# Kernel optimization log

Measured on AMD Instinct MI355X. Metric: run time of the kernel, lower is better.

The kernel has to match this reference:

```python
import jax, jax.numpy as jnp
import numpy as np

B, S, H = 32, 4096, 16
QC, LORA, ROPE, NOPE, VH, DM = 1536, 512, 64, 128, 128, 2048
SCALE = 1.0 / np.sqrt(NOPE + ROPE)


def _rope(x, pos):
    # GPT-NeoX style rotary, dim=ROPE, base=10000. x: [B,H,ROPE] or [B,ROPE]
    half = ROPE // 2
    inv = 1.0 / (10000.0 ** (jnp.arange(half, dtype=jnp.float32) / half))
    f = pos.astype(jnp.float32)[:, None] * inv  # [B, half]
    cos, sin = jnp.cos(f), jnp.sin(f)
    if x.ndim == 3:
        cos, sin = cos[:, None, :], sin[:, None, :]
    x1, x2 = x[..., :half], x[..., half:]
    return jnp.concatenate([x1 * cos - x2 * sin, x2 * cos + x1 * sin], axis=-1)


def setup_inputs() -> dict:
    key = jax.random.key(0)
    ks = jax.random.split(key, 11)
    w = 0.02  # small init so logits are well-scaled
    return {
        "q_c": jax.random.normal(ks[0], (B, QC), jnp.float32),
        "k_c_normed": jax.random.normal(ks[1], (B, LORA), jnp.float32),
        "k_pe": jax.random.normal(ks[2], (B, ROPE), jnp.float32),
        "kv_c_cache": jax.random.normal(ks[3], (B, S, LORA), jnp.float32),
        "k_pe_cache": jax.random.normal(ks[4], (B, S, ROPE), jnp.float32),
        "W_UQ": jax.random.normal(ks[5], (QC, H, NOPE), jnp.float32) * w,
        "W_UK": jax.random.normal(ks[6], (LORA, H, NOPE), jnp.float32) * w,
        "W_QR": jax.random.normal(ks[7], (QC, H * ROPE), jnp.float32) * w,
        "W_UV": jax.random.normal(ks[8], (LORA, H, VH), jnp.float32) * w,
        "W_O": jax.random.normal(ks[9], (H * VH, DM), jnp.float32) * w,
        "input_positions": jnp.full((B,), S - 1, dtype=jnp.int32),
    }


def reference(q_c, k_c_normed, k_pe, kv_c_cache, k_pe_cache,
              W_UQ, W_UK, W_QR, W_UV, W_O, input_positions):
    pos = input_positions
    # matrix-absorbed q_nope: (q_c @ W_UQ) absorbed through W_UK -> latent space
    q_t = jnp.einsum('bd,dhn->bhn', q_c, W_UQ)            # [B,H,NOPE]
    q_nope = jnp.einsum('bhn,lhn->bhl', q_t, W_UK)        # [B,H,LORA]
    q_pe = _rope((q_c @ W_QR).reshape(B, H, ROPE), pos)   # [B,H,ROPE]
    k_pe_rot = _rope(k_pe, pos)                            # [B,ROPE]
    # write current latent token into cache (paged write flattened)
    b_idx = jnp.arange(B)
    kv_c = kv_c_cache.at[b_idx, pos].set(k_c_normed)       # [B,S,LORA]
    kp = k_pe_cache.at[b_idx, pos].set(k_pe_rot)           # [B,S,ROPE]
    # attention in latent space
    scores = (jnp.einsum('bhl,bsl->bhs', q_nope, kv_c)
              + jnp.einsum('bhr,bsr->bhs', q_pe, kp)) * SCALE
    attn = jax.nn.softmax(scores, axis=-1)                 # [B,H,S]
    o = jnp.einsum('bhs,bsl->bhl', attn, kv_c)             # [B,H,LORA]
    v = jnp.einsum('bhl,lhv->bhv', o, W_UV)                # [B,H,VH]
    out = v.reshape(B, H * VH) @ W_O                       # [B,DM]
    return out.reshape(B, 1, DM)
```

## Files before the change

kernel.cpp:

```cpp
#include <hip/hip_runtime.h>
#include <hip/hip_bf16.h>
#include <math.h>

#define B 32
#define S 4096
#define H 16
#define QC 1536
#define LORA 512
#define ROPE 64
#define NOPE 128
#define VH 128
#define DM 2048
#define NC 32
#define CHUNK (S / NC)
#define TR 8
#define NT (CHUNK / TR)
#define NKS 24

__device__ __constant__ float SCALE_C = 0.07216878364870323f;

__global__ __launch_bounds__(256) void k_proj_part(
    const float* __restrict__ q_c, const float* __restrict__ W_UQ,
    const float* __restrict__ W_QR, float* __restrict__ part) {
    const int ks = blockIdx.x, cs = blockIdx.y, t = threadIdx.x;
    const int k0 = ks * 64;
    __shared__ float qs[64][32];
    for (int i = t; i < 64 * 32; i += 256) {
        const int k = i >> 5, b2 = i & 31;
        qs[k][b2] = q_c[(size_t)b2 * QC + k0 + k];
    }
    __syncthreads();
    const int tc = t & 63, tb = t >> 6;
    const int col = cs * 256 + tc * 4;
    const float* W; int N, coll;
    if (cs < 8) { W = W_UQ; N = 2048; coll = col; }
    else        { W = W_QR; N = 1024; coll = col - 2048; }
    float4 acc[8];
#pragma unroll
    for (int i = 0; i < 8; i++) acc[i] = make_float4(0.f, 0.f, 0.f, 0.f);
#pragma unroll 4
    for (int k = 0; k < 64; ++k) {
        const float4 w4 = *(const float4*)(W + (size_t)(k0 + k) * N + coll);
        const float4 a1 = *(const float4*)&qs[k][tb * 8];
        const float4 a2 = *(const float4*)&qs[k][tb * 8 + 4];
        acc[0].x += a1.x * w4.x; acc[0].y += a1.x * w4.y; acc[0].z += a1.x * w4.z; acc[0].w += a1.x * w4.w;
        acc[1].x += a1.y * w4.x; acc[1].y += a1.y * w4.y; acc[1].z += a1.y * w4.z; acc[1].w += a1.y * w4.w;
        acc[2].x += a1.z * w4.x; acc[2].y += a1.z * w4.y; acc[2].z += a1.z * w4.z; acc[2].w += a1.z * w4.w;
        acc[3].x += a1.w * w4.x; acc[3].y += a1.w * w4.y; acc[3].z += a1.w * w4.z; acc[3].w += a1.w * w4.w;
        acc[4].x += a2.x * w4.x; acc[4].y += a2.x * w4.y; acc[4].z += a2.x * w4.z; acc[4].w += a2.x * w4.w;
        acc[5].x += a2.y * w4.x; acc[5].y += a2.y * w4.y; acc[5].z += a2.y * w4.z; acc[5].w += a2.y * w4.w;
        acc[6].x += a2.z * w4.x; acc[6].y += a2.z * w4.y; acc[6].z += a2.z * w4.z; acc[6].w += a2.z * w4.w;
        acc[7].x += a2.w * w4.x; acc[7].y += a2.w * w4.y; acc[7].z += a2.w * w4.z; acc[7].w += a2.w * w4.w;
    }
#pragma unroll
    for (int j = 0; j < 8; j++) {
        const int b2 = tb * 8 + j;
        *(float4*)(part + ((size_t)ks * 32 + b2) * 3072 + col) = acc[j];
    }
}

__global__ void k_proj_reduce(const float* __restrict__ part, float* __restrict__ q_t,
                              float* __restrict__ qr) {
    const int idx = blockIdx.x * 256 + threadIdx.x;
    const int b = idx / 768, c4 = idx % 768;
    const int col = c4 * 4;
    float4 acc = make_float4(0.f, 0.f, 0.f, 0.f);
    for (int ks = 0; ks < NKS; ks++) {
        const float4 p = *(const float4*)(part + ((size_t)ks * 32 + b) * 3072 + col);
        acc.x += p.x; acc.y += p.y; acc.z += p.z; acc.w += p.w;
    }
    if (col < 2048) *(float4*)(q_t + (size_t)b * 2048 + col) = acc;
    else            *(float4*)(qr + (size_t)b * 1024 + col - 2048) = acc;
}

__global__ void k_rope(const float* __restrict__ qr, const float* __restrict__ k_pe,
                       const int* __restrict__ pos_arr, float* __restrict__ q_pe,
                       float* __restrict__ kpe_rot) {
    const int b = blockIdx.x, t = threadIdx.x;
    const int pos = pos_arr[b];
    for (int p = t; p < (H + 1) * 32; p += 256) {
        const int j = p & 31;
        const int grp = p >> 5;
        const double inv = pow(10000.0, -(double)j / 32.0);
        const double f = (double)pos * inv;
        const float c = (float)cos(f), s = (float)sin(f);
        if (grp < H) {
            const float* x = qr + (size_t)b * 1024 + grp * 64;
            float* o = q_pe + (size_t)b * 1024 + grp * 64;
            const float x1 = x[j], x2 = x[j + 32];
            o[j] = x1 * c - x2 * s;
            o[j + 32] = x2 * c + x1 * s;
        } else {
            const float* x = k_pe + (size_t)b * 64;
            float* o = kpe_rot + (size_t)b * 64;
            const float x1 = x[j], x2 = x[j + 32];
            o[j] = x1 * c - x2 * s;
            o[j + 32] = x2 * c + x1 * s;
        }
    }
}

__global__ __launch_bounds__(256) void k_qnope(
    const float* __restrict__ q_t, const float* __restrict__ W_UK,
    float* __restrict__ q_nope) {
    const int l0 = blockIdx.x * 64, b0 = blockIdx.y * 4, h = blockIdx.z;
    const int t = threadIdx.x;
    __shared__ float qs[4][NOPE];
    for (int i = t; i < 4 * NOPE; i += 256) {
        const int b2 = i >> 7, n = i & 127;
        qs[b2][n] = q_t[(size_t)(b0 + b2) * 2048 + h * NOPE + n];
    }
    __syncthreads();
    const int wave = t >> 6, lane = t & 63;
    const int half = lane >> 5, nl = (lane & 31) * 4;
    for (int sw = 0; sw < 8; ++sw) {
        const int l = l0 + sw * 8 + wave * 2 + half;
        const float4 w4 = *(const float4*)(W_UK + ((size_t)l * H + h) * NOPE + nl);
#pragma unroll
        for (int b2 = 0; b2 < 4; ++b2) {
            const float4 a4 = *(const float4*)&qs[b2][nl];
            float d = a4.x * w4.x + a4.y * w4.y + a4.z * w4.z + a4.w * w4.w;
            d += __shfl_xor(d, 16);
            d += __shfl_xor(d, 8);
            d += __shfl_xor(d, 4);
            d += __shfl_xor(d, 2);
            d += __shfl_xor(d, 1);
            if ((lane & 31) == 0)
                q_nope[((size_t)(b0 + b2) * H + h) * LORA + l] = d;
        }
    }
}

__global__ __launch_bounds__(256) void k_flash(
    const float* __restrict__ q_nope, const float* __restrict__ q_pe,
    const float* __restrict__ kv_cache, const float* __restrict__ kpe_cache,
    const float* __restrict__ k_c_normed, const float* __restrict__ kpe_rot,
    const int* __restrict__ pos_arr, float* __restrict__ part_o,
    float* __restrict__ part_ml) {
    __shared__ float lds_kv[2][TR][LORA];
    __shared__ float lds_pe[2][TR][ROPE];
    const int blk = blockIdx.x;
    const int b = blk / NC, c = blk % NC;
    const int t = threadIdx.x;
    const int g = t >> 4, j = t & 15;
    const int wave = t >> 6, lane = t & 63;
    const int pos = pos_arr[b];
    const int s0 = c * CHUNK;
    const int rel = pos - s0;
    const int ptile = (rel >= 0 && rel < CHUNK) ? (rel / TR) : -1;

    const char* kvg = (const char*)kv_cache + (size_t)b * S * LORA * 4;
    const char* peg = (const char*)kpe_cache + (size_t)b * S * ROPE * 4;
    const float* kc_b = k_c_normed + (size_t)b * LORA;
    const float* kr_b = kpe_rot + (size_t)b * ROPE;

    const int wo = wave * 1024 + lane * 16;

    auto stage = [&](int bi, int tile) {
        const char* gk = kvg + (size_t)(s0 + tile * TR) * (LORA * 4);
        char* lk = (char*)&lds_kv[bi][0][0];
#pragma unroll
        for (int i = 0; i < 4; ++i) {
            __builtin_amdgcn_global_load_lds(
                (const __attribute__((address_space(1))) void*)(gk + i * 4096 + wo),
                (__attribute__((address_space(3))) void*)(lk + i * 4096 + wave * 1024),
                16, 0, 0);
        }
        if (t < 128) {
            const char* gp = peg + (size_t)(s0 + tile * TR) * (ROPE * 4);
            char* lp = (char*)&lds_pe[bi][0][0];
            __builtin_amdgcn_global_load_lds(
                (const __attribute__((address_space(1))) void*)(gp + wo),
                (__attribute__((address_space(3))) void*)(lp + wave * 1024),
                16, 0, 0);
        }
    };
    auto patch = [&](int bi, int prow) {
        if (t < 128)
            ((float4*)&lds_kv[bi][prow][0])[t] = ((const float4*)kc_b)[t];
        else if (t < 144)
            ((float4*)&lds_pe[bi][prow][0])[t - 128] = ((const float4*)kr_b)[t - 128];
    };

    float4 q4[9];
    const float* qn = q_nope + ((size_t)b * H + g) * LORA;
#pragma unroll
    for (int k = 0; k < 8; k++) q4[k] = *(const float4*)(qn + 4 * j + 64 * k);
    q4[8] = *(const float4*)(q_pe + ((size_t)b * H + g) * 64 + 4 * j);

    float m_run = -INFINITY, l_run = 0.f;
    float4 o_acc[8];
#pragma unroll
    for (int k = 0; k < 8; k++) o_acc[k] = make_float4(0.f, 0.f, 0.f, 0.f);

    stage(0, 0);
    asm volatile("s_waitcnt vmcnt(0)" ::: "memory");
    __syncthreads();
    if (ptile == 0) { patch(0, rel); __syncthreads(); }

    int cur = 0;
    for (int tile = 0; tile < NT; ++tile) {
        if (tile + 1 < NT) stage(cur ^ 1, tile + 1);

        for (int r = 0; r < TR; ++r) {
            const float* kvr = &lds_kv[cur][r][0];
            float4 kv4[8];
#pragma unroll
            for (int k = 0; k < 8; k++) kv4[k] = *(const float4*)(kvr + 4 * j + 64 * k);
            float4 p4 = *(const float4*)(&lds_pe[cur][r][0] + 4 * j);

            float acc = 0.f;
#pragma unroll
            for (int k = 0; k < 8; k++)
                acc += q4[k].x * kv4[k].x + q4[k].y * kv4[k].y +
                       q4[k].z * kv4[k].z + q4[k].w * kv4[k].w;
            acc += q4[8].x * p4.x + q4[8].y * p4.y + q4[8].z * p4.z + q4[8].w * p4.w;
            acc += __shfl_xor(acc, 8);
            acc += __shfl_xor(acc, 4);
            acc += __shfl_xor(acc, 2);
            acc += __shfl_xor(acc, 1);
            const float sc = acc * SCALE_C;

            if (sc > m_run + 8.0f) {
                const float alpha = __expf(m_run - sc);
                l_run *= alpha;
#pragma unroll
                for (int k = 0; k < 8; k++) {
                    o_acc[k].x *= alpha; o_acc[k].y *= alpha;
                    o_acc[k].z *= alpha; o_acc[k].w *= alpha;
                }
                m_run = sc;
            }
            const float p = __expf(sc - m_run);
            l_run += p;
#pragma unroll
            for (int k = 0; k < 8; k++) {
                o_acc[k].x += p * kv4[k].x; o_acc[k].y += p * kv4[k].y;
                o_acc[k].z += p * kv4[k].z; o_acc[k].w += p * kv4[k].w;
            }
        }

        asm volatile("s_waitcnt vmcnt(0)" ::: "memory");
        __syncthreads();
        if (tile + 1 < NT && ptile == tile + 1) {
            patch(cur ^ 1, rel - ptile * TR);
            __syncthreads();
        }
        cur ^= 1;
    }

    float* po = part_o + (((size_t)b * NC + c) * H + g) * LORA;
#pragma unroll
    for (int k = 0; k < 8; k++) *(float4*)(po + 4 * j + 64 * k) = o_acc[k];
    if (j == 0) {
        float* pml = part_ml + (((size_t)b * NC + c) * H + g) * 2;
        pml[0] = m_run;
        pml[1] = l_run;
    }
}

__global__ __launch_bounds__(256) void k_combine(
    const float* __restrict__ part_o, const float* __restrict__ part_ml,
    const float* __restrict__ W_UV, float* __restrict__ v) {
    const int b0 = blockIdx.x * 4, h = blockIdx.y, t = threadIdx.x;
    __shared__ float ml_s[4][NC][2];
    __shared__ float o_s[4][LORA];
    if (t < 256) {
        const int b2 = t >> 6, c = (t >> 1) & 31, w = t & 1;
        ml_s[b2][c][w] = part_ml[(((size_t)(b0 + b2) * NC + c) * H + h) * 2 + w];
    }
    __syncthreads();
    float m_b[4], inv_l[4];
#pragma unroll
    for (int b2 = 0; b2 < 4; ++b2) {
        float m = -INFINITY;
        for (int c = 0; c < NC; c++) m = fmaxf(m, ml_s[b2][c][0]);
        float l = 0.f;
        for (int c = 0; c < NC; c++) l += ml_s[b2][c][1] * __expf(ml_s[b2][c][0] - m);
        m_b[b2] = m;
        inv_l[b2] = 1.0f / l;
    }
    for (int i = t; i < 4 * LORA; i += 256) {
        const int b2 = i >> 9, li = i & 511;
        float acc = 0.f;
        for (int c = 0; c < NC; c++) {
            acc += part_o[(((size_t)(b0 + b2) * NC + c) * H + h) * LORA + li] *
                   __expf(ml_s[b2][c][0] - m_b[b2]);
        }
        o_s[b2][li] = acc * inv_l[b2];
    }
    __syncthreads();
    const int vi = t & 127, bp = t >> 7;
    float acc0 = 0.f, acc1 = 0.f;
    for (int l = 0; l < LORA; l += 4) {
        const float w0 = W_UV[(size_t)(l + 0) * (H * VH) + h * VH + vi];
        const float w1 = W_UV[(size_t)(l + 1) * (H * VH) + h * VH + vi];
        const float w2 = W_UV[(size_t)(l + 2) * (H * VH) + h * VH + vi];
        const float w3 = W_UV[(size_t)(l + 3) * (H * VH) + h * VH + vi];
        const float4 oa = *(const float4*)&o_s[bp * 2][l];
        const float4 ob = *(const float4*)&o_s[bp * 2 + 1][l];
        acc0 += oa.x * w0 + oa.y * w1 + oa.z * w2 + oa.w * w3;
        acc1 += ob.x * w0 + ob.y * w1 + ob.z * w2 + ob.w * w3;
    }
    v[(size_t)(b0 + bp * 2) * (H * VH) + h * VH + vi] = acc0;
    v[(size_t)(b0 + bp * 2 + 1) * (H * VH) + h * VH + vi] = acc1;
}

__global__ void k_out(const float* __restrict__ v, const float* __restrict__ W_O,
                      float* __restrict__ out_part) {
    const int dsl = blockIdx.x, ksl = blockIdx.y, t = threadIdx.x;
    const int d0 = dsl * 128, k0 = ksl * 128;
    __shared__ float vs[32][128];
    for (int i = t; i < 32 * 128; i += 256) {
        const int bi = i >> 7, kk = i & 127;
        vs[bi][kk] = v[(size_t)bi * DM + k0 + kk];
    }
    __syncthreads();
    const int dl = t & 127, bh = t >> 7;
    float acc[16];
#pragma unroll
    for (int i = 0; i < 16; i++) acc[i] = 0.f;
    for (int kk = 0; kk < 128; kk += 4) {
        const float w0 = W_O[(size_t)(k0 + kk + 0) * DM + d0 + dl];
        const float w1 = W_O[(size_t)(k0 + kk + 1) * DM + d0 + dl];
        const float w2 = W_O[(size_t)(k0 + kk + 2) * DM + d0 + dl];
        const float w3 = W_O[(size_t)(k0 + kk + 3) * DM + d0 + dl];
#pragma unroll
        for (int i = 0; i < 16; i++) {
            const float4 vv = *(const float4*)&vs[bh * 16 + i][kk];
            acc[i] += vv.x * w0 + vv.y * w1 + vv.z * w2 + vv.w * w3;
        }
    }
    float* op = out_part + (size_t)ksl * 32 * DM;
#pragma unroll
    for (int i = 0; i < 16; i++) op[(size_t)(bh * 16 + i) * DM + d0 + dl] = acc[i];
}

__global__ void k_out_reduce(const float* __restrict__ out_part, float* __restrict__ out) {
    const int idx = blockIdx.x * 256 + threadIdx.x;
    float4 acc = make_float4(0.f, 0.f, 0.f, 0.f);
    for (int ks = 0; ks < 16; ks++) {
        float4 p = *(const float4*)(out_part + (size_t)ks * (32 * DM) + (size_t)idx * 4);
        acc.x += p.x; acc.y += p.y; acc.z += p.z; acc.w += p.w;
    }
    *(float4*)(out + (size_t)idx * 4) = acc;
}

extern "C" void kernel_launch(void* const* d_in, const int* in_sizes, int n_in,
                              void* d_out, int out_size, void* d_ws, size_t ws_size,
                              hipStream_t stream) {
    const float* q_c        = (const float*)d_in[0];
    const float* k_c_normed = (const float*)d_in[1];
    const float* k_pe       = (const float*)d_in[2];
    const float* kv_c_cache = (const float*)d_in[3];
    const float* k_pe_cache = (const float*)d_in[4];
    const float* W_UQ       = (const float*)d_in[5];
    const float* W_UK       = (const float*)d_in[6];
    const float* W_QR       = (const float*)d_in[7];
    const float* W_UV       = (const float*)d_in[8];
    const float* W_O        = (const float*)d_in[9];
    const int*   pos        = (const int*)d_in[10];

    float* ws = (float*)d_ws;
    float* q_t      = ws;
    float* qr       = q_t + 65536;
    float* q_pe     = qr + 32768;
    float* kpe_rot  = q_pe + 32768;
    float* q_nope   = kpe_rot + 2048;
    float* part_o   = q_nope + 262144;
    float* part_ml  = part_o + (size_t)B * NC * H * LORA;
    float* v        = part_ml + (size_t)B * NC * H * 2;
    float* out_part = v + 65536;
    float* proj_part = out_part + (size_t)16 * 32 * DM;

    k_proj_part<<<dim3(NKS, 12), 256, 0, stream>>>(q_c, W_UQ, W_QR, proj_part);
    k_proj_reduce<<<96, 256, 0, stream>>>(proj_part, q_t, qr);
    k_rope<<<32, 256, 0, stream>>>(qr, k_pe, pos, q_pe, kpe_rot);
    k_qnope<<<dim3(8, 8, 16), 256, 0, stream>>>(q_t, W_UK, q_nope);
    k_flash<<<B * NC, 256, 0, stream>>>(q_nope, q_pe, kv_c_cache, k_pe_cache,
                                        k_c_normed, kpe_rot, pos, part_o, part_ml);
    k_combine<<<dim3(8, 16), 256, 0, stream>>>(part_o, part_ml, W_UV, v);
    k_out<<<dim3(16, 16), 256, 0, stream>>>(v, W_O, out_part);
    k_out_reduce<<<64, 256, 0, stream>>>(out_part, (float*)d_out);
}
```

Before: 231.0 us.

## Remap flash-attention threads so each wave handles four heads over the full latent row

Each thread previously owned one head and a 36-float slice, re-reading 9 float4s from LDS per row for every head group. Now each wave owns four heads and each lane holds 8 latent values plus one rope value, so every KV row value read from LDS is reused across four heads. This cuts LDS read traffic per row roughly fourfold. The cost is a full 64-lane shuffle reduction (6 steps times 4 heads) instead of a 16-lane one, and more per-thread state for softmax.

Measured after the change: 274.8 us. 1.19x slower.

```diff
diff --git a/kernel.cpp b/kernel.cpp
--- a/kernel.cpp
+++ b/kernel.cpp
@@ -142,8 +142,8 @@
     const int blk = blockIdx.x;
     const int b = blk / NC, c = blk % NC;
     const int t = threadIdx.x;
-    const int g = t >> 4, j = t & 15;
     const int wave = t >> 6, lane = t & 63;
+    const int l4 = lane * 4;
     const int pos = pos_arr[b];
     const int s0 = c * CHUNK;
     const int rel = pos - s0;
@@ -182,16 +182,24 @@
             ((float4*)&lds_pe[bi][prow][0])[t - 128] = ((const float4*)kr_b)[t - 128];
     };
 
-    float4 q4[9];
-    const float* qn = q_nope + ((size_t)b * H + g) * LORA;
-#pragma unroll
-    for (int k = 0; k < 8; k++) q4[k] = *(const float4*)(qn + 4 * j + 64 * k);
-    q4[8] = *(const float4*)(q_pe + ((size_t)b * H + g) * 64 + 4 * j);
-
-    float m_run = -INFINITY, l_run = 0.f;
-    float4 o_acc[8];
-#pragma unroll
-    for (int k = 0; k < 8; k++) o_acc[k] = make_float4(0.f, 0.f, 0.f, 0.f);
+    float4 q0[4], q1[4];
+    float qp[4];
+#pragma unroll
+    for (int h = 0; h < 4; ++h) {
+        const float* qn = q_nope + ((size_t)b * H + wave * 4 + h) * LORA;
+        q0[h] = *(const float4*)(qn + l4);
+        q1[h] = *(const float4*)(qn + 256 + l4);
+        qp[h] = q_pe[((size_t)b * H + wave * 4 + h) * 64 + lane];
+    }
+
+    float m_run[4], l_run[4];
+    float4 o0[4], o1[4];
+#pragma unroll
+    for (int h = 0; h < 4; ++h) {
+        m_run[h] = -INFINITY; l_run[h] = 0.f;
+        o0[h] = make_float4(0.f, 0.f, 0.f, 0.f);
+        o1[h] = make_float4(0.f, 0.f, 0.f, 0.f);
+    }
 
     stage(0, 0);
     asm volatile("s_waitcnt vmcnt(0)" ::: "memory");
@@ -203,40 +211,38 @@
         if (tile + 1 < NT) stage(cur ^ 1, tile + 1);
 
         for (int r = 0; r < TR; ++r) {
-            const float* kvr = &lds_kv[cur][r][0];
-            float4 kv4[8];
-#pragma unroll
-            for (int k = 0; k < 8; k++) kv4[k] = *(const float4*)(kvr + 4 * j + 64 * k);
-            float4 p4 = *(const float4*)(&lds_pe[cur][r][0] + 4 * j);
-
-            float acc = 0.f;
-#pragma unroll
-            for (int k = 0; k < 8; k++)
-                acc += q4[k].x * kv4[k].x + q4[k].y * kv4[k].y +
-                       q4[k].z * kv4[k].z + q4[k].w * kv4[k].w;
-            acc += q4[8].x * p4.x + q4[8].y * p4.y + q4[8].z * p4.z + q4[8].w * p4.w;
-            acc += __shfl_xor(acc, 8);
-            acc += __shfl_xor(acc, 4);
-            acc += __shfl_xor(acc, 2);
-            acc += __shfl_xor(acc, 1);
-            const float sc = acc * SCALE_C;
-
-            if (sc > m_run + 8.0f) {
-                const float alpha = __expf(m_run - sc);
-                l_run *= alpha;
-#pragma unroll
-                for (int k = 0; k < 8; k++) {
-                    o_acc[k].x *= alpha; o_acc[k].y *= alpha;
-                    o_acc[k].z *= alpha; o_acc[k].w *= alpha;
+            const float4 k0 = *(const float4*)&lds_kv[cur][r][l4];
+            const float4 k1 = *(const float4*)&lds_kv[cur][r][256 + l4];
+            const float  kp = lds_pe[cur][r][lane];
+
+            float sc[4];
+#pragma unroll
+            for (int h = 0; h < 4; ++h) {
+                sc[h] = q0[h].x * k0.x + q0[h].y * k0.y + q0[h].z * k0.z + q0[h].w * k0.w
+                      + q1[h].x * k1.x + q1[h].y * k1.y + q1[h].z * k1.z + q1[h].w * k1.w
+                      + qp[h] * kp;
+            }
+#pragma unroll
+            for (int msk = 32; msk >= 1; msk >>= 1) {
+#pragma unroll
+                for (int h = 0; h < 4; ++h) sc[h] += __shfl_xor(sc[h], msk);
+            }
+#pragma unroll
+            for (int h = 0; h < 4; ++h) {
+                const float s = sc[h] * SCALE_C;
+                if (s > m_run[h] + 8.0f) {
+                    const float alpha = __expf(m_run[h] - s);
+                    l_run[h] *= alpha;
+                    o0[h].x *= alpha; o0[h].y *= alpha; o0[h].z *= alpha; o0[h].w *= alpha;
+                    o1[h].x *= alpha; o1[h].y *= alpha; o1[h].z *= alpha; o1[h].w *= alpha;
+                    m_run[h] = s;
                 }
-                m_run = sc;
-            }
-            const float p = __expf(sc - m_run);
-            l_run += p;
-#pragma unroll
-            for (int k = 0; k < 8; k++) {
-                o_acc[k].x += p * kv4[k].x; o_acc[k].y += p * kv4[k].y;
-                o_acc[k].z += p * kv4[k].z; o_acc[k].w += p * kv4[k].w;
+                const float p = __expf(s - m_run[h]);
+                l_run[h] += p;
+                o0[h].x += p * k0.x; o0[h].y += p * k0.y;
+                o0[h].z += p * k0.z; o0[h].w += p * k0.w;
+                o1[h].x += p * k1.x; o1[h].y += p * k1.y;
+                o1[h].z += p * k1.z; o1[h].w += p * k1.w;
             }
         }
 
@@ -249,13 +255,20 @@
         cur ^= 1;
     }
 
-    float* po = part_o + (((size_t)b * NC + c) * H + g) * LORA;
-#pragma unroll
-    for (int k = 0; k < 8; k++) *(float4*)(po + 4 * j + 64 * k) = o_acc[k];
-    if (j == 0) {
-        float* pml = part_ml + (((size_t)b * NC + c) * H + g) * 2;
-        pml[0] = m_run;
-        pml[1] = l_run;
+    float* po = part_o + (((size_t)b * NC + c) * H) * LORA;
+#pragma unroll
+    for (int h = 0; h < 4; ++h) {
+        float* p = po + (size_t)(wave * 4 + h) * LORA;
+        *(float4*)(p + l4) = o0[h];
+        *(float4*)(p + 256 + l4) = o1[h];
+    }
+    if (lane == 0) {
+        float* pml = part_ml + (((size_t)b * NC + c) * H + wave * 4) * 2;
+#pragma unroll
+        for (int h = 0; h < 4; ++h) {
+            pml[2 * h] = m_run[h];
+            pml[2 * h + 1] = l_run[h];
+        }
     }
 }
 
```

## Process two heads per thread group in flash kernel with 128-thread blocks

Applied to the files above, without the earlier changes.

Halves the flash-decode block to 128 threads and has each 16-lane group handle two heads, so every KV row loaded from LDS feeds two dot products and two output accumulations. Staging loops are adjusted so the smaller block still loads each tile. This cuts LDS read traffic per head, but roughly doubles per-thread register use (two q vectors and two accumulators), which can lower occupancy or cause spills.

Result: faster. 214.8 us (-7.0%).

```diff
diff --git a/kernel.cpp b/kernel.cpp
--- a/kernel.cpp
+++ b/kernel.cpp
@@ -131,7 +131,7 @@
     }
 }
 
-__global__ __launch_bounds__(256) void k_flash(
+__global__ __launch_bounds__(128) void k_flash(
     const float* __restrict__ q_nope, const float* __restrict__ q_pe,
     const float* __restrict__ kv_cache, const float* __restrict__ kpe_cache,
     const float* __restrict__ k_c_normed, const float* __restrict__ kpe_rot,
@@ -160,38 +160,40 @@
         const char* gk = kvg + (size_t)(s0 + tile * TR) * (LORA * 4);
         char* lk = (char*)&lds_kv[bi][0][0];
 #pragma unroll
-        for (int i = 0; i < 4; ++i) {
+        for (int i = 0; i < 8; ++i) {
             __builtin_amdgcn_global_load_lds(
-                (const __attribute__((address_space(1))) void*)(gk + i * 4096 + wo),
-                (__attribute__((address_space(3))) void*)(lk + i * 4096 + wave * 1024),
+                (const __attribute__((address_space(1))) void*)(gk + i * 2048 + wo),
+                (__attribute__((address_space(3))) void*)(lk + i * 2048 + wave * 1024),
                 16, 0, 0);
         }
-        if (t < 128) {
-            const char* gp = peg + (size_t)(s0 + tile * TR) * (ROPE * 4);
-            char* lp = (char*)&lds_pe[bi][0][0];
-            __builtin_amdgcn_global_load_lds(
-                (const __attribute__((address_space(1))) void*)(gp + wo),
-                (__attribute__((address_space(3))) void*)(lp + wave * 1024),
-                16, 0, 0);
-        }
+        const char* gp = peg + (size_t)(s0 + tile * TR) * (ROPE * 4);
+        char* lp = (char*)&lds_pe[bi][0][0];
+        __builtin_amdgcn_global_load_lds(
+            (const __attribute__((address_space(1))) void*)(gp + wo),
+            (__attribute__((address_space(3))) void*)(lp + wave * 1024),
+            16, 0, 0);
     };
     auto patch = [&](int bi, int prow) {
-        if (t < 128)
-            ((float4*)&lds_kv[bi][prow][0])[t] = ((const float4*)kc_b)[t];
-        else if (t < 144)
-            ((float4*)&lds_pe[bi][prow][0])[t - 128] = ((const float4*)kr_b)[t - 128];
+        ((float4*)&lds_kv[bi][prow][0])[t] = ((const float4*)kc_b)[t];
+        if (t < 16)
+            ((float4*)&lds_pe[bi][prow][0])[t] = ((const float4*)kr_b)[t];
     };
 
-    float4 q4[9];
-    const float* qn = q_nope + ((size_t)b * H + g) * LORA;
-#pragma unroll
-    for (int k = 0; k < 8; k++) q4[k] = *(const float4*)(qn + 4 * j + 64 * k);
-    q4[8] = *(const float4*)(q_pe + ((size_t)b * H + g) * 64 + 4 * j);
-
-    float m_run = -INFINITY, l_run = 0.f;
-    float4 o_acc[8];
-#pragma unroll
-    for (int k = 0; k < 8; k++) o_acc[k] = make_float4(0.f, 0.f, 0.f, 0.f);
+    float4 q4[2][9];
+#pragma unroll
+    for (int h = 0; h < 2; ++h) {
+        const float* qn = q_nope + ((size_t)b * H + 2 * g + h) * LORA;
+#pragma unroll
+        for (int k = 0; k < 8; k++) q4[h][k] = *(const float4*)(qn + 4 * j + 64 * k);
+        q4[h][8] = *(const float4*)(q_pe + ((size_t)b * H + 2 * g + h) * 64 + 4 * j);
+    }
+
+    float m_run[2] = {-INFINITY, -INFINITY}, l_run[2] = {0.f, 0.f};
+    float4 o_acc[2][8];
+#pragma unroll
+    for (int h = 0; h < 2; ++h)
+#pragma unroll
+        for (int k = 0; k < 8; k++) o_acc[h][k] = make_float4(0.f, 0.f, 0.f, 0.f);
 
     stage(0, 0);
     asm volatile("s_waitcnt vmcnt(0)" ::: "memory");
@@ -209,34 +211,43 @@
             for (int k = 0; k < 8; k++) kv4[k] = *(const float4*)(kvr + 4 * j + 64 * k);
             float4 p4 = *(const float4*)(&lds_pe[cur][r][0] + 4 * j);
 
-            float acc = 0.f;
-#pragma unroll
-            for (int k = 0; k < 8; k++)
-                acc += q4[k].x * kv4[k].x + q4[k].y * kv4[k].y +
-                       q4[k].z * kv4[k].z + q4[k].w * kv4[k].w;
-            acc += q4[8].x * p4.x + q4[8].y * p4.y + q4[8].z * p4.z + q4[8].w * p4.w;
-            acc += __shfl_xor(acc, 8);
-            acc += __shfl_xor(acc, 4);
-            acc += __shfl_xor(acc, 2);
-            acc += __shfl_xor(acc, 1);
-            const float sc = acc * SCALE_C;
-
-            if (sc > m_run + 8.0f) {
-                const float alpha = __expf(m_run - sc);
-                l_run *= alpha;
+            float sc[2];
+#pragma unroll
+            for (int h = 0; h < 2; ++h) {
+                float acc = 0.f;
+#pragma unroll
+                for (int k = 0; k < 8; k++)
+                    acc += q4[h][k].x * kv4[k].x + q4[h][k].y * kv4[k].y +
+                           q4[h][k].z * kv4[k].z + q4[h][k].w * kv4[k].w;
+                acc += q4[h][8].x * p4.x + q4[h][8].y * p4.y +
+                       q4[h][8].z * p4.z + q4[h][8].w * p4.w;
+                sc[h] = acc;
+            }
+#pragma unroll
+            for (int msk = 8; msk >= 1; msk >>= 1) {
+                sc[0] += __shfl_xor(sc[0], msk);
+                sc[1] += __shfl_xor(sc[1], msk);
+            }
+#pragma unroll
+            for (int h = 0; h < 2; ++h) {
+                const float s = sc[h] * SCALE_C;
+                if (s > m_run[h] + 8.0f) {
+                    const float alpha = __expf(m_run[h] - s);
+                    l_run[h] *= alpha;
+#pragma unroll
+                    for (int k = 0; k < 8; k++) {
+                        o_acc[h][k].x *= alpha; o_acc[h][k].y *= alpha;
+                        o_acc[h][k].z *= alpha; o_acc[h][k].w *= alpha;
+                    }
+                    m_run[h] = s;
+                }
+                const float p = __expf(s - m_run[h]);
+                l_run[h] += p;
 #pragma unroll
                 for (int k = 0; k < 8; k++) {
-                    o_acc[k].x *= alpha; o_acc[k].y *= alpha;
-                    o_acc[k].z *= alpha; o_acc[k].w *= alpha;
+                    o_acc[h][k].x += p * kv4[k].x; o_acc[h][k].y += p * kv4[k].y;
+                    o_acc[h][k].z += p * kv4[k].z; o_acc[h][k].w += p * kv4[k].w;
                 }
-                m_run = sc;
-            }
-            const float p = __expf(sc - m_run);
-            l_run += p;
-#pragma unroll
-            for (int k = 0; k < 8; k++) {
-                o_acc[k].x += p * kv4[k].x; o_acc[k].y += p * kv4[k].y;
-                o_acc[k].z += p * kv4[k].z; o_acc[k].w += p * kv4[k].w;
             }
         }
 
@@ -249,13 +260,17 @@
         cur ^= 1;
     }
 
-    float* po = part_o + (((size_t)b * NC + c) * H + g) * LORA;
-#pragma unroll
-    for (int k = 0; k < 8; k++) *(float4*)(po + 4 * j + 64 * k) = o_acc[k];
+    float* po = part_o + (((size_t)b * NC + c) * H) * LORA;
+#pragma unroll
+    for (int h = 0; h < 2; ++h) {
+        float* p = po + (size_t)(2 * g + h) * LORA;
+#pragma unroll
+        for (int k = 0; k < 8; k++) *(float4*)(p + 4 * j + 64 * k) = o_acc[h][k];
+    }
     if (j == 0) {
-        float* pml = part_ml + (((size_t)b * NC + c) * H + g) * 2;
-        pml[0] = m_run;
-        pml[1] = l_run;
+        float* pml = part_ml + (((size_t)b * NC + c) * H + 2 * g) * 2;
+        pml[0] = m_run[0]; pml[1] = l_run[0];
+        pml[2] = m_run[1]; pml[3] = l_run[1];
     }
 }
 
@@ -377,7 +392,7 @@
     k_proj_reduce<<<96, 256, 0, stream>>>(proj_part, q_t, qr);
     k_rope<<<32, 256, 0, stream>>>(qr, k_pe, pos, q_pe, kpe_rot);
     k_qnope<<<dim3(8, 8, 16), 256, 0, stream>>>(q_t, W_UK, q_nope);
-    k_flash<<<B * NC, 256, 0, stream>>>(q_nope, q_pe, kv_c_cache, k_pe_cache,
+    k_flash<<<B * NC, 128, 0, stream>>>(q_nope, q_pe, kv_c_cache, k_pe_cache,
                                         k_c_normed, kpe_rot, pos, part_o, part_ml);
     k_combine<<<dim3(8, 16), 256, 0, stream>>>(part_o, part_ml, W_UV, v);
     k_out<<<dim3(16, 16), 256, 0, stream>>>(v, W_O, out_part);
```
